# Optimization experiments

Measured on AMD Instinct MI355X. Metric: run time of the kernel, lower is better.

The kernel has to match this reference:

```python
import jax, jax.numpy as jnp
import numpy as np

CONF = 0.25      # confidence threshold (module default)
IOU = 0.45       # NMS IoU threshold (class attribute)
TOPK = 1000      # fixed candidate budget (jit-friendly stand-in for boolean filtering)
MAX_WH = 4096.0  # class offset so NMS is per-class (YOLOv5 trick)


def xywh2xyxy(b):
    xy, wh = b[..., :2], b[..., 2:4]
    return jnp.concatenate([xy - wh * 0.5, xy + wh * 0.5], axis=-1)


def box_iou(a, b):
    # a: [K,4] xyxy, b: [K,4] xyxy -> [K,K]
    lt = jnp.maximum(a[:, None, :2], b[None, :, :2])
    rb = jnp.minimum(a[:, None, 2:], b[None, :, 2:])
    wh = jnp.clip(rb - lt, 0.0)
    inter = wh[..., 0] * wh[..., 1]
    area_a = (a[:, 2] - a[:, 0]) * (a[:, 3] - a[:, 1])
    area_b = (b[:, 2] - b[:, 0]) * (b[:, 3] - b[:, 1])
    return inter / (area_a[:, None] + area_b[None, :] - inter + 1e-9)


def nms_single(pred):
    # pred: [N, 5+C] = (xywh, obj, cls scores)
    boxes = xywh2xyxy(pred[:, :4])
    obj = pred[:, 4]
    cls = pred[:, 5:]
    cls_conf = jnp.max(cls, axis=-1)
    cls_id = jnp.argmax(cls, axis=-1)
    score = obj * cls_conf                       # conf = obj_conf * cls_conf
    masked = jnp.where(score > CONF, score, -1.0)
    top_scores, idx = jax.lax.top_k(masked, TOPK)  # sorted descending
    boxes_k = boxes[idx]                          # [K,4]
    cls_k = cls_id[idx].astype(boxes.dtype)       # [K]
    valid_k = top_scores > CONF                   # candidates passing threshold
    # per-class NMS via coordinate offset
    off = boxes_k + cls_k[:, None] * MAX_WH
    iou = box_iou(off, off)
    iou = iou * (1.0 - jnp.eye(TOPK, dtype=iou.dtype))  # ignore self-IoU
    # greedy suppression in descending score order
    def step(suppressed, i):
        keep_i = jnp.logical_and(jnp.logical_not(suppressed[i]), valid_k[i])
        suppressed = jnp.logical_or(suppressed, jnp.logical_and(keep_i, iou[i] > IOU))
        return suppressed, keep_i
    _, keep = jax.lax.scan(step, jnp.zeros(TOPK, dtype=bool), jnp.arange(TOPK))
    det = jnp.concatenate([boxes_k, top_scores[:, None], cls_k[:, None]], axis=-1)  # [K,6]
    return jnp.where(keep[:, None], det, 0.0)


def setup_inputs() -> dict:
    key = jax.random.key(0)
    x = jax.random.uniform(key, (8, 25200, 85), dtype=jnp.float32)
    return {"x": x}


def reference(x):
    # [B, K, 6] detections (xyxy, conf, cls); suppressed/invalid rows zeroed.
    return jax.vmap(nms_single)(x)
```

## Files before the change

kernel.cpp:

```cpp
#include <hip/hip_runtime.h>
#include <stdint.h>

#define NB 8
#define NPRED 25200
#define NTOP 1000
#define NCLS 80
#define CONF_T 0.25f
#define IOU_THR 0.45f
#define MAXWH 4096.0f
#define NKEYS 2048
#define NBINSF 4096
#define FSH 12
#define FBASE 0x3E800
#define SBLK 128
#define SBPB 197

typedef unsigned long long u64;

__device__ __forceinline__ u64 shfl_u64(u64 v, int src) {
    int lo = __shfl((int)(unsigned)v, src);
    int hi = __shfl((int)(unsigned)(v >> 32), src);
    return ((u64)(unsigned)hi << 32) | (unsigned)lo;
}

__global__ __launch_bounds__(256) void k_score(const float* __restrict__ x,
                                               float* __restrict__ msc,
                                               int* __restrict__ cls) {
#pragma clang fp contract(off)
    __shared__ __align__(16) float sm[SBLK * 85];
    const int b = blockIdx.x / SBPB;
    const int blk = blockIdx.x % SBPB;
    const int t = threadIdx.x;
    const int wave = t >> 6, lane = t & 63;
    const long long TOT4 = (long long)NB * NPRED * 85 / 4;
    const long long base4 = ((long long)b * NPRED + (long long)blk * SBLK) * 85 / 4;
    const float4* x4 = (const float4*)x;
    const int tile4 = SBLK * 85 / 4;

    for (int k = 0; k < 11; ++k) {
        int ib = k * 256 + wave * 64;
        int fi = ib + lane;
        if (fi < tile4) {
            long long gi = base4 + fi;
            if (gi >= TOT4) gi = TOT4 - 1;
            __builtin_amdgcn_global_load_lds(
                (const __attribute__((address_space(1))) void*)(x4 + gi),
                (__attribute__((address_space(3))) void*)(sm + (size_t)ib * 4),
                16, 0, 0);
        }
    }
    __syncthreads();

    const int p = t >> 1;
    const int h = t & 1;
    const int pred = blk * SBLK + p;
    const float* rowp = &sm[p * 85];
    float obj = rowp[4];
    const int cb = 5 + h * 40;
    float best = rowp[cb];
    int bid = h * 40;
    for (int c = 1; c < 40; ++c) {
        float v = rowp[cb + c];
        if (v > best) { best = v; bid = h * 40 + c; }
    }
    float obest = __shfl_xor(best, 1);
    int obid = __shfl_xor(bid, 1);
    if (h == 0 && pred < NPRED) {
        float fb = best; int fc = bid;
        if (obest > fb) { fb = obest; fc = obid; }
        float score = obj * fb;
        int q = b * NPRED + pred;
        msc[q] = (score > CONF_T) ? score : -1.0f;
        cls[q] = fc;
    }
}

__global__ __launch_bounds__(1024) void k_fused(const float* __restrict__ x,
                                                const float* __restrict__ msc,
                                                const int* __restrict__ cls,
                                                float* __restrict__ out) {
#pragma clang fp contract(off)
    __shared__ __align__(16) unsigned char uni[NKEYS * 8];
    __shared__ __align__(16) unsigned hh[NBINSF];
    __shared__ unsigned wtot[16];
    __shared__ __align__(16) float4 obx[NTOP];
    __shared__ float oco[NTOP];
    __shared__ float osc[NTOP];
    __shared__ int   ocl[NTOP];
    __shared__ int ovf;
    u64* keys = (u64*)uni;
    const int b = blockIdx.x, t = threadIdx.x;
    const int wave = t >> 6, lane = t & 63;
    const float* ms = msc + (size_t)b * NPRED;

    float sv[25];
#pragma unroll
    for (int k = 0; k < 25; ++k) {
        int p = t + k * 1024;
        sv[k] = (p < NPRED) ? ms[p] : -1.0f;
    }

    ((uint4*)hh)[t] = make_uint4(0u, 0u, 0u, 0u);
    if (t == 0) ovf = 0;
    __syncthreads();

#pragma unroll
    for (int k = 0; k < 25; ++k) {
        float s = sv[k];
        if (s > CONF_T) {
            unsigned bits = __float_as_uint(s);
            int bin = (int)(bits >> FSH) - FBASE;
            bin = bin < 0 ? 0 : (bin > NBINSF - 1 ? NBINSF - 1 : bin);
            atomicAdd(&hh[bin], 1u);
        }
    }
    __syncthreads();

    uint4 hc = ((const uint4*)hh)[t];
    unsigned psum = hc.x + hc.y + hc.z + hc.w;
    unsigned v = psum;
    for (int d = 1; d < 64; d <<= 1) {
        unsigned o = __shfl_down(v, d);
        if (lane + d < 64) v += o;
    }
    if (lane == 0) wtot[wave] = v;
    keys[t] = ~0ULL; keys[t + 1024] = ~0ULL;
    __syncthreads();
    unsigned after = 0;
    for (int w2 = wave + 1; w2 < 16; ++w2) after += wtot[w2];
    unsigned exclSuf = after + (v - psum);
    unsigned o3 = exclSuf;
    unsigned o2 = o3 + hc.w;
    unsigned o1 = o2 + hc.z;
    unsigned o0 = o1 + hc.y;
    ((uint4*)hh)[t] = make_uint4(o0, o1, o2, o3);
    __syncthreads();

#pragma unroll
    for (int k = 0; k < 25; ++k) {
        float s = sv[k];
        if (s > CONF_T) {
            unsigned bits = __float_as_uint(s);
            int bin = (int)(bits >> FSH) - FBASE;
            bin = bin < 0 ? 0 : (bin > NBINSF - 1 ? NBINSF - 1 : bin);
            unsigned slot = atomicAdd(&hh[bin], 1u);
            if (slot < (unsigned)NKEYS)
                keys[slot] = ((u64)(~bits) << 32) | (unsigned)(t + k * 1024);
        }
    }
    __syncthreads();

    auto binOf = [](u64 kk) -> int {
        unsigned bits = ~(unsigned)(kk >> 32);
        int bin = (int)(bits >> FSH) - FBASE;
        return bin < 0 ? 0 : (bin > NBINSF - 1 ? NBINSF - 1 : bin);
    };
#pragma unroll
    for (int pp = 0; pp < 2; ++pp) {
        int p = t + pp * 1024;
        u64 k0 = keys[p];
        if (k0 == ~0ULL) continue;
        int mybin = binOf(k0);
        bool head = (p == 0) || (keys[p - 1] == ~0ULL) || (binOf(keys[p - 1]) != mybin);
        if (!head) continue;
        int e = p + 1;
        while (e < NKEYS) {
            u64 kn = keys[e];
            if (kn == ~0ULL || binOf(kn) != mybin) break;
            ++e;
        }
        for (int i2 = p + 1; i2 < e; ++i2) {
            u64 kv = keys[i2];
            int j2 = i2 - 1;
            while (j2 >= p && keys[j2] > kv) { keys[j2 + 1] = keys[j2]; --j2; }
            keys[j2 + 1] = kv;
        }
    }
    __syncthreads();

    if (t < NTOP) {
        u64 key = keys[t];
        unsigned p = (unsigned)key;
        float score = __uint_as_float(~(unsigned)(key >> 32));
        bool vd = score > CONF_T;
        float4 o = make_float4(0.f, 0.f, 0.f, 0.f);
        float co = 0.f; int cid = -1;
        if (vd) {
            const float* xp = x + ((size_t)b * NPRED + p) * 85;
            float xc = xp[0], yc = xp[1], w = xp[2], h = xp[3];
            float hw = w * 0.5f, hh2 = h * 0.5f;
            o.x = xc - hw; o.y = yc - hh2; o.z = xc + hw; o.w = yc + hh2;
            cid = cls[(size_t)b * NPRED + p];
            co = (float)cid * MAXWH;
        }
        obx[t] = o; oco[t] = co; osc[t] = score; ocl[t] = cid;
    }
    __syncthreads();

    u64* bm = (u64*)uni;
    unsigned char* sup = uni + 10240;
    for (int i = t; i < NCLS * 16; i += 1024) bm[i] = 0;
    if (t < NTOP) sup[t] = 0;
    __syncthreads();
    if (t < NTOP && ocl[t] >= 0)
        atomicOr(&bm[ocl[t] * 16 + (t >> 6)], 1ull << (t & 63));
    __syncthreads();

    {
        for (int c2 = wave; c2 < NCLS; c2 += 16) {
            u64 w = (lane < 16) ? bm[c2 * 16 + lane] : 0ull;
            int cum = 0, myw = -1, rem = 0;
            u64 myword = 0;
#pragma unroll
            for (int ww = 0; ww < 16; ++ww) {
                u64 wv = shfl_u64(w, ww);
                int pc = __popcll(wv);
                if (myw < 0 && lane < cum + pc) { myw = ww; rem = lane - cum; myword = wv; }
                cum += pc;
            }
            int n2 = cum;
            if (n2 == 0) continue;
            if (n2 > 64) { ovf = 1; continue; }
            bool active = (lane < n2);
            int rank = 0;
            float ax1v = 0.f, ay1v = 0.f, ax2v = 0.f, ay2v = 0.f, arv = 0.f;
            if (active) {
                int pos = 0, r = rem;
#pragma unroll
                for (int wd = 32; wd >= 1; wd >>= 1) {
                    u64 mask = ((1ull << wd) - 1ull) << pos;
                    int cc = __popcll(myword & mask);
                    if (r >= cc) { r -= cc; pos += wd; }
                }
                rank = myw * 64 + pos;
                float4 A = obx[rank]; float cA = oco[rank];
                ax1v = A.x + cA; ay1v = A.y + cA;
                ax2v = A.z + cA; ay2v = A.w + cA;
                arv = (ax2v - ax1v) * (ay2v - ay1v);
            }
            u64 alive = (n2 >= 64) ? ~0ull : ((1ull << n2) - 1ull);
            u64 kept = 0;
            while (alive) {
                int i = (int)__builtin_ctzll(alive);
                u64 bit = 1ull << i;
                kept |= bit;
                float bx1 = __shfl(ax1v, i), by1 = __shfl(ay1v, i);
                float bx2 = __shfl(ax2v, i), by2 = __shfl(ay2v, i);
                float bar = __shfl(arv, i);
                float ltx = fmaxf(bx1, ax1v), lty = fmaxf(by1, ay1v);
                float rbx = fminf(bx2, ax2v), rby = fminf(by2, ay2v);
                float ww2 = fmaxf(rbx - ltx, 0.0f), hh3 = fmaxf(rby - lty, 0.0f);
                float inter = ww2 * hh3;
                float iou = inter / (((bar + arv) - inter) + 1e-9f);
                u64 suppr = __ballot(iou > IOU_THR);
                alive &= ~(suppr | bit);
            }
            if (active) sup[rank] = ((kept >> lane) & 1ull) ? 0 : 1;
        }
    }
    __syncthreads();

    if (ovf && t == 0) {
        for (int c2 = 0; c2 < NCLS; ++c2) {
            int n2 = 0;
            for (int w2 = 0; w2 < 16; ++w2) n2 += __popcll(bm[c2 * 16 + w2]);
            if (n2 <= 64) continue;
            for (int a2 = 0; a2 < NTOP; ++a2) {
                if (ocl[a2] != c2 || sup[a2]) continue;
                float4 A = obx[a2]; float cA = oco[a2];
                float ax1 = A.x + cA, ay1 = A.y + cA;
                float ax2 = A.z + cA, ay2 = A.w + cA;
                float areaA = (ax2 - ax1) * (ay2 - ay1);
                for (int d2 = a2 + 1; d2 < NTOP; ++d2) {
                    if (ocl[d2] != c2 || sup[d2]) continue;
                    float4 Bb = obx[d2];
                    float bx1 = Bb.x + cA, by1 = Bb.y + cA;
                    float bx2 = Bb.z + cA, by2 = Bb.w + cA;
                    float ltx = fmaxf(ax1, bx1), lty = fmaxf(ay1, by1);
                    float rbx = fminf(ax2, bx2), rby = fminf(ay2, by2);
                    float ww = fmaxf(rbx - ltx, 0.0f), hh3 = fmaxf(rby - lty, 0.0f);
                    float inter = ww * hh3;
                    float areaB = (bx2 - bx1) * (by2 - by1);
                    float iou = inter / (((areaA + areaB) - inter) + 1e-9f);
                    if (iou > IOU_THR) sup[d2] = 1;
                }
            }
        }
    }
    __syncthreads();

    if (t < NTOP) {
        bool keep = (ocl[t] >= 0) && (sup[t] == 0);
        float4 o = obx[t];
        size_t d6 = ((size_t)b * NTOP + t) * 6;
        out[d6 + 0] = keep ? o.x : 0.0f;
        out[d6 + 1] = keep ? o.y : 0.0f;
        out[d6 + 2] = keep ? o.z : 0.0f;
        out[d6 + 3] = keep ? o.w : 0.0f;
        out[d6 + 4] = keep ? osc[t] : 0.0f;
        out[d6 + 5] = keep ? (float)ocl[t] : 0.0f;
    }
}

extern "C" void kernel_launch(void* const* d_in, const int* in_sizes, int n_in,
                              void* d_out, int out_size, void* d_ws, size_t ws_size,
                              hipStream_t stream) {
    const float* x = (const float*)d_in[0];
    char* ws = (char*)d_ws;
    float* msc = (float*)(ws);
    int* cls = (int*)(ws + 806400);

    k_score<<<NB * SBPB, 256, 0, stream>>>(x, msc, cls);
    k_fused<<<NB, 1024, 0, stream>>>(x, msc, cls, (float*)d_out);
}
```

Baseline: 145.0 us.

## Replace fine histogram plus insertion sort with coarse bins, threshold bin, and rank sort

Top-k selection now uses a coarser 1025-bin histogram scanned by a single wave, which also finds the cutoff bin holding the 1000th score. Only keys at or above that bin are scattered. Each key then gets its position by counting smaller keys inside its bin and is written straight to a separate sorted array. This replaces the serial per-bin insertion sort done by bin-head threads. Bitmap and suppression-flag initialisation are merged into the gather step, removing one barrier. The cost is quadratic work inside any crowded bin, since the coarser bins hold more keys.

New measurement: 129.2 us. 1.12x faster.

```diff
diff --git a/kernel.cpp b/kernel.cpp
--- a/kernel.cpp
+++ b/kernel.cpp
@@ -8,10 +8,8 @@
 #define CONF_T 0.25f
 #define IOU_THR 0.45f
 #define MAXWH 4096.0f
-#define NKEYS 2048
-#define NBINSF 4096
-#define FSH 12
-#define FBASE 0x3E800
+#define CAP 2048
+#define NBINS 1025
 #define SBLK 128
 #define SBPB 197
 
@@ -80,17 +78,18 @@
                                                 const int* __restrict__ cls,
                                                 float* __restrict__ out) {
 #pragma clang fp contract(off)
-    __shared__ __align__(16) unsigned char uni[NKEYS * 8];
-    __shared__ __align__(16) unsigned hh[NBINSF];
-    __shared__ unsigned wtot[16];
+    __shared__ __align__(16) unsigned char uni[CAP * 8];
+    __shared__ unsigned hh[NBINS];
+    __shared__ unsigned hbase[NBINS];
+    __shared__ __align__(16) u64 ksort[NTOP];
     __shared__ __align__(16) float4 obx[NTOP];
     __shared__ float oco[NTOP];
     __shared__ float osc[NTOP];
     __shared__ int   ocl[NTOP];
+    __shared__ int sB;
     __shared__ int ovf;
     u64* keys = (u64*)uni;
     const int b = blockIdx.x, t = threadIdx.x;
-    const int wave = t >> 6, lane = t & 63;
     const float* ms = msc + (size_t)b * NPRED;
 
     float sv[25];
@@ -100,8 +99,10 @@
         sv[k] = (p < NPRED) ? ms[p] : -1.0f;
     }
 
-    ((uint4*)hh)[t] = make_uint4(0u, 0u, 0u, 0u);
-    if (t == 0) ovf = 0;
+    for (int i = t; i < NBINS; i += 1024) hh[i] = 0;
+    keys[t] = ~0ULL; keys[t + 1024] = ~0ULL;
+    if (t < NTOP) ksort[t] = ~0ULL;
+    if (t == 0) { ovf = 0; sB = 0; }
     __syncthreads();
 
 #pragma unroll
@@ -109,77 +110,94 @@
         float s = sv[k];
         if (s > CONF_T) {
             unsigned bits = __float_as_uint(s);
-            int bin = (int)(bits >> FSH) - FBASE;
-            bin = bin < 0 ? 0 : (bin > NBINSF - 1 ? NBINSF - 1 : bin);
+            int bin = (int)(bits >> 14) - 0xFA00;
+            bin = bin < 0 ? 0 : (bin > 1024 ? 1024 : bin);
             atomicAdd(&hh[bin], 1u);
         }
     }
     __syncthreads();
 
-    uint4 hc = ((const uint4*)hh)[t];
-    unsigned psum = hc.x + hc.y + hc.z + hc.w;
-    unsigned v = psum;
-    for (int d = 1; d < 64; d <<= 1) {
-        unsigned o = __shfl_down(v, d);
-        if (lane + d < 64) v += o;
-    }
-    if (lane == 0) wtot[wave] = v;
-    keys[t] = ~0ULL; keys[t + 1024] = ~0ULL;
-    __syncthreads();
-    unsigned after = 0;
-    for (int w2 = wave + 1; w2 < 16; ++w2) after += wtot[w2];
-    unsigned exclSuf = after + (v - psum);
-    unsigned o3 = exclSuf;
-    unsigned o2 = o3 + hc.w;
-    unsigned o1 = o2 + hc.z;
-    unsigned o0 = o1 + hc.y;
-    ((uint4*)hh)[t] = make_uint4(o0, o1, o2, o3);
-    __syncthreads();
+    if (t < 64) {
+        const int lane = t;
+        const int hi2 = 1024 - 16 * lane;
+        unsigned lc[16];
+        unsigned sum = 0;
+#pragma unroll
+        for (int k = 0; k < 16; ++k) { lc[k] = hh[hi2 - k]; sum += lc[k]; }
+        if (lane == 63) sum += hh[0];
+        unsigned v = sum;
+        for (int d = 1; d < 64; d <<= 1) {
+            unsigned o = __shfl_up(v, d);
+            if (lane >= d) v += o;
+        }
+        unsigned excl = v - sum;
+        unsigned run = excl;
+#pragma unroll
+        for (int k = 0; k < 16; ++k) { hbase[hi2 - k] = run; run += lc[k]; }
+        if (lane == 63) hbase[0] = run;
+        u64 ball = __ballot(v >= NTOP);
+        int B = 0;
+        if (ball != 0) {
+            int sel = __builtin_ctzll(ball);
+            if (lane == sel) {
+                unsigned r2 = excl;
+                for (int k = 0; k < 16; ++k) {
+                    r2 += lc[k];
+                    if (r2 >= NTOP) { B = hi2 - k; break; }
+                }
+            }
+            B = __shfl(B, sel);
+        }
+        if (lane == 0) sB = B;
+    }
+    __syncthreads();
+    const int B = sB;
 
 #pragma unroll
     for (int k = 0; k < 25; ++k) {
         float s = sv[k];
         if (s > CONF_T) {
             unsigned bits = __float_as_uint(s);
-            int bin = (int)(bits >> FSH) - FBASE;
-            bin = bin < 0 ? 0 : (bin > NBINSF - 1 ? NBINSF - 1 : bin);
-            unsigned slot = atomicAdd(&hh[bin], 1u);
-            if (slot < (unsigned)NKEYS)
-                keys[slot] = ((u64)(~bits) << 32) | (unsigned)(t + k * 1024);
-        }
-    }
-    __syncthreads();
-
-    auto binOf = [](u64 kk) -> int {
-        unsigned bits = ~(unsigned)(kk >> 32);
-        int bin = (int)(bits >> FSH) - FBASE;
-        return bin < 0 ? 0 : (bin > NBINSF - 1 ? NBINSF - 1 : bin);
-    };
-#pragma unroll
-    for (int pp = 0; pp < 2; ++pp) {
-        int p = t + pp * 1024;
-        u64 k0 = keys[p];
-        if (k0 == ~0ULL) continue;
-        int mybin = binOf(k0);
-        bool head = (p == 0) || (keys[p - 1] == ~0ULL) || (binOf(keys[p - 1]) != mybin);
-        if (!head) continue;
-        int e = p + 1;
-        while (e < NKEYS) {
-            u64 kn = keys[e];
-            if (kn == ~0ULL || binOf(kn) != mybin) break;
-            ++e;
-        }
-        for (int i2 = p + 1; i2 < e; ++i2) {
-            u64 kv = keys[i2];
-            int j2 = i2 - 1;
-            while (j2 >= p && keys[j2] > kv) { keys[j2 + 1] = keys[j2]; --j2; }
-            keys[j2 + 1] = kv;
-        }
-    }
-    __syncthreads();
-
+            int bin = (int)(bits >> 14) - 0xFA00;
+            bin = bin < 0 ? 0 : (bin > 1024 ? 1024 : bin);
+            if (bin >= B) {
+                unsigned slot = atomicAdd(&hbase[bin], 1u);
+                if (slot < (unsigned)CAP)
+                    keys[slot] = ((u64)(~bits) << 32) | (unsigned)(t + k * 1024);
+            }
+        }
+    }
+    __syncthreads();
+
+    {
+        auto binOf = [](u64 kk) -> int {
+            unsigned bits = ~(unsigned)(kk >> 32);
+            int bin = (int)(bits >> 14) - 0xFA00;
+            return bin < 0 ? 0 : (bin > 1024 ? 1024 : bin);
+        };
+#pragma unroll
+        for (int pp = 0; pp < 2; ++pp) {
+            int i = t + pp * 1024;
+            u64 my = keys[i];
+            if (my == ~0ULL) continue;
+            int bin = binOf(my);
+            int e2 = (int)hbase[bin];
+            if (e2 > CAP) e2 = CAP;
+            int base = e2 - (int)hh[bin];
+            if (base < 0) base = 0;
+            unsigned r = (unsigned)base;
+            for (int j = base; j < e2; ++j) r += (keys[j] < my) ? 1u : 0u;
+            if (r < (unsigned)NTOP) ksort[r] = my;
+        }
+    }
+    __syncthreads();
+
+    u64* bm = (u64*)uni;
+    unsigned char* sup = uni + 10240;
+    for (int i = t; i < NCLS * 16; i += 1024) bm[i] = 0;
     if (t < NTOP) {
-        u64 key = keys[t];
+        sup[t] = 0;
+        u64 key = ksort[t];
         unsigned p = (unsigned)key;
         float score = __uint_as_float(~(unsigned)(key >> 32));
         bool vd = score > CONF_T;
@@ -196,17 +214,12 @@
         obx[t] = o; oco[t] = co; osc[t] = score; ocl[t] = cid;
     }
     __syncthreads();
-
-    u64* bm = (u64*)uni;
-    unsigned char* sup = uni + 10240;
-    for (int i = t; i < NCLS * 16; i += 1024) bm[i] = 0;
-    if (t < NTOP) sup[t] = 0;
-    __syncthreads();
     if (t < NTOP && ocl[t] >= 0)
         atomicOr(&bm[ocl[t] * 16 + (t >> 6)], 1ull << (t & 63));
     __syncthreads();
 
     {
+        const int wave = t >> 6, lane = t & 63;
         for (int c2 = wave; c2 < NCLS; c2 += 16) {
             u64 w = (lane < 16) ? bm[c2 * 16 + lane] : 0ull;
             int cum = 0, myw = -1, rem = 0;
```
